# Kernel tuning notes

Measured on AMD Instinct MI355X. Metric: run time of the kernel, lower is better.

The kernel has to match this reference:

```python
import jax, jax.numpy as jnp
import numpy as np

B, D1, T = 256, 512, 256   # batch, input features, time steps
O1, O2 = 256, 128          # output features, output time/classes


def setup_inputs() -> dict:
    key = jax.random.key(0)
    ks = jax.random.split(key, 5)
    x = jax.random.normal(ks[0], (B, D1, T), dtype=jnp.float32)
    W1 = jax.random.normal(ks[1], (O1, D1), dtype=jnp.float32) / np.sqrt(D1).astype(np.float32)
    W = jax.random.normal(ks[2], (T, T), dtype=jnp.float32) / np.sqrt(T).astype(np.float32)
    W2 = jax.random.normal(ks[3], (T, O2), dtype=jnp.float32) / np.sqrt(T).astype(np.float32)
    alpha = jnp.array([0.5], dtype=jnp.float32)
    bias = jax.random.normal(ks[4], (O1, O2), dtype=jnp.float32) * 0.01
    return {"x": x, "W1": W1, "W": W, "W2": W2, "alpha": alpha, "bias": bias}


def reference(x, W1, W, W2, alpha, bias):
    # mode-1 product: project features. E: [B, O1, T]
    E = jnp.einsum('od,bdt->bot', W1, x)
    # temporal attention: softmax over time of E @ W. A: [B, O1, T]
    A = jax.nn.softmax(jnp.einsum('bot,ts->bos', E, W), axis=-1)
    a = alpha[0]
    blended = a * E + (1.0 - a) * E * A
    # mode-2 product: project time axis, add bias. Y: [B, O1, O2]
    Y = jnp.einsum('bot,ts->bos', blended, W2) + bias
    # per-sample softmax over the output-feature axis (torch.softmax(item4[i], 0))
    return jax.nn.softmax(Y, axis=1)
```

## Files before the change

### kernel.cpp

```cpp
#include <hip/hip_runtime.h>
#include <hip/hip_bf16.h>
#include <math.h>

#define B_   256
#define D1_  512
#define T_   256
#define O1_  256
#define O2_  128
#define OT   64

typedef __attribute__((ext_vector_type(8))) _Float16 f16x8;
typedef __attribute__((ext_vector_type(4))) float f32x4;

__device__ inline unsigned pkh2(float a, float b) {
    union { _Float16 h[2]; unsigned u; } c;
    c.h[0] = (_Float16)a; c.h[1] = (_Float16)b; return c.u;
}
__device__ inline uint2 cvth4(float v0, float v1, float v2, float v3) {
    uint2 r; r.x = pkh2(v0, v1); r.y = pkh2(v2, v3); return r;
}
__device__ inline f16x8 cvt8h(const float* v) {
    f16x8 r;
    #pragma unroll
    for (int j = 0; j < 8; ++j) r[j] = (_Float16)v[j];
    return r;
}
__device__ inline f16x8 ld16(const char* p) {
    union { uint2 a[2]; f16x8 v; } f;
    f.a[0] = *(const uint2*)p;
    f.a[1] = *(const uint2*)(p + 8);
    return f.v;
}
__device__ inline f16x8 ldb128(const char* p) { return *(const f16x8*)p; }

#define MFMAH __builtin_amdgcn_mfma_f32_16x16x32_f16

__global__ __launch_bounds__(512, 4) void tabl_mfma(
    const float* __restrict__ x, const float* __restrict__ W1,
    const float* __restrict__ W, const float* __restrict__ W2,
    const float* __restrict__ alpha, const float* __restrict__ bias,
    float* __restrict__ out)
{
    __shared__ __align__(16) char Eh[OT * 512];
    __shared__ __align__(16) char Bst[2][256 * 72];
    __shared__ float redm[4][OT];
    __shared__ float reds[4][OT];

    const int tid    = threadIdx.x;
    const int lane16 = tid & 15;
    const int lg     = (tid >> 4) & 3;
    const int wid    = tid >> 6;
    const int wm     = wid >> 2;
    const int wn     = wid & 3;

    const int bid = blockIdx.x;
    const int idx = bid >> 3;
    const int b     = (bid & 7) + 8 * (idx >> 2);
    const int obase = (idx & 3) * OT;

    const int xs_t  = tid & 255;
    const int xs_kh = tid >> 8;
    const int stO   = xs_t * 72 + xs_kh * 32;
    const int zs = tid & 127, zq = (tid >> 7) & 3;
    const int stZ   = zs * 72 + zq * 16;

    const int rArow[2] = { obase + wm * 32 + lane16, obase + wm * 32 + 16 + lane16 };
    const int eR[2]    = { wm * 32 + lane16, wm * 32 + 16 + lane16 };
    const int eBase[2] = { eR[0] * 512, eR[1] * 512 };
    const int eSw[2]   = { (eR[0] & 7) << 4, (eR[1] & 7) << 4 };
    int bOff[4], b3Off[2];
    #pragma unroll
    for (int nt = 0; nt < 4; ++nt) bOff[nt] = (wn * 64 + nt * 16 + lane16) * 72 + lg * 16;
    #pragma unroll
    for (int nt = 0; nt < 2; ++nt) b3Off[nt] = (wn * 32 + nt * 16 + lane16) * 72 + lg * 16;

    f32x4 Eacc[2][4];
    #pragma unroll
    for (int mt = 0; mt < 2; ++mt)
        #pragma unroll
        for (int nt = 0; nt < 4; ++nt) Eacc[mt][nt] = (f32x4){0.f,0.f,0.f,0.f};

    const float* xcol = x + (size_t)b * (D1_ * T_) + xs_t;
    float xn[16];
    f16x8 AhC[2];

    {
        float x0[16];
        #pragma unroll
        for (int j = 0; j < 16; ++j) x0[j] = xcol[(size_t)(xs_kh * 16 + j) * T_];
        #pragma unroll
        for (int mt = 0; mt < 2; ++mt) {
            float av[8];
            *(float4*)&av[0] = *(const float4*)(W1 + (size_t)rArow[mt] * D1_ + lg * 8);
            *(float4*)&av[4] = *(const float4*)(W1 + (size_t)rArow[mt] * D1_ + lg * 8 + 4);
            AhC[mt] = cvt8h(av);
        }
        #pragma unroll
        for (int q = 0; q < 4; ++q)
            *(uint2*)(Bst[0] + stO + q * 8) = cvth4(x0[q*4+0], x0[q*4+1], x0[q*4+2], x0[q*4+3]);
    }
    __syncthreads();

    #pragma unroll 2
    for (int c = 0; c < 16; ++c) {
        const int cur = c & 1;
        if (c < 15) {
            #pragma unroll
            for (int j = 0; j < 16; ++j)
                xn[j] = xcol[(size_t)((c + 1) * 32 + xs_kh * 16 + j) * T_];
        }
        float4 apN[2][2];
        if (c < 15) {
            #pragma unroll
            for (int mt = 0; mt < 2; ++mt) {
                const float4* ap = (const float4*)(W1 + (size_t)rArow[mt] * D1_ + (c + 1) * 32 + lg * 8);
                apN[mt][0] = ap[0]; apN[mt][1] = ap[1];
            }
        }
        __builtin_amdgcn_s_setprio(1);
        #pragma unroll
        for (int nt = 0; nt < 4; ++nt) {
            f16x8 Bh = ld16(Bst[cur] + bOff[nt]);
            #pragma unroll
            for (int mt = 0; mt < 2; ++mt)
                Eacc[mt][nt] = MFMAH(AhC[mt], Bh, Eacc[mt][nt], 0,0,0);
        }
        __builtin_amdgcn_s_setprio(0);
        if (c < 15) {
            #pragma unroll
            for (int q = 0; q < 4; ++q)
                *(uint2*)(Bst[cur^1] + stO + q * 8) = cvth4(xn[q*4+0], xn[q*4+1], xn[q*4+2], xn[q*4+3]);
            #pragma unroll
            for (int mt = 0; mt < 2; ++mt) {
                float av[8];
                *(float4*)&av[0] = apN[mt][0];
                *(float4*)&av[4] = apN[mt][1];
                AhC[mt] = cvt8h(av);
            }
        }
        __syncthreads();
    }

    #pragma unroll
    for (int mt = 0; mt < 2; ++mt)
        #pragma unroll
        for (int nt = 0; nt < 4; ++nt)
            #pragma unroll
            for (int i = 0; i < 4; ++i) {
                int r = wm * 32 + mt * 16 + lg * 4 + i;
                int t = wn * 64 + nt * 16 + lane16;
                union { _Float16 h; unsigned short u; } cc;
                cc.h = (_Float16)Eacc[mt][nt][i];
                *(unsigned short*)(Eh + r * 512 + ((2 * t) ^ ((r & 7) << 4))) = cc.u;
            }

    f32x4 Sacc[2][4];
    #pragma unroll
    for (int mt = 0; mt < 2; ++mt)
        #pragma unroll
        for (int nt = 0; nt < 4; ++nt) Sacc[mt][nt] = (f32x4){0.f,0.f,0.f,0.f};

    const float* wcol = W + xs_t;
    {
        float w0[16];
        #pragma unroll
        for (int j = 0; j < 16; ++j) w0[j] = wcol[(size_t)(xs_kh * 16 + j) * T_];
        #pragma unroll
        for (int q = 0; q < 4; ++q)
            *(uint2*)(Bst[0] + stO + q * 8) = cvth4(w0[q*4+0], w0[q*4+1], w0[q*4+2], w0[q*4+3]);
    }
    __syncthreads();

    float wv[16];
    #pragma unroll 2
    for (int c = 0; c < 8; ++c) {
        const int cur = c & 1;
        if (c < 7) {
            #pragma unroll
            for (int j = 0; j < 16; ++j)
                wv[j] = wcol[(size_t)((c + 1) * 32 + xs_kh * 16 + j) * T_];
        }
        f16x8 Af[2];
        #pragma unroll
        for (int mt = 0; mt < 2; ++mt)
            Af[mt] = ldb128(Eh + eBase[mt] + ((c * 64 + lg * 16) ^ eSw[mt]));
        __builtin_amdgcn_s_setprio(1);
        #pragma unroll
        for (int nt = 0; nt < 4; ++nt) {
            f16x8 Bf = ld16(Bst[cur] + bOff[nt]);
            #pragma unroll
            for (int mt = 0; mt < 2; ++mt)
                Sacc[mt][nt] = MFMAH(Af[mt], Bf, Sacc[mt][nt], 0,0,0);
        }
        __builtin_amdgcn_s_setprio(0);
        if (c < 7) {
            #pragma unroll
            for (int q = 0; q < 4; ++q)
                *(uint2*)(Bst[cur^1] + stO + q * 8) = cvth4(wv[q*4+0], wv[q*4+1], wv[q*4+2], wv[q*4+3]);
        }
        __syncthreads();
    }

    const float a_ = alpha[0];
    float pm[2][4];
    #pragma unroll
    for (int mt = 0; mt < 2; ++mt)
        #pragma unroll
        for (int i = 0; i < 4; ++i) {
            float m = fmaxf(fmaxf(Sacc[mt][0][i], Sacc[mt][1][i]),
                            fmaxf(Sacc[mt][2][i], Sacc[mt][3][i]));
            m = fmaxf(m, __shfl_xor(m, 1));
            m = fmaxf(m, __shfl_xor(m, 2));
            m = fmaxf(m, __shfl_xor(m, 4));
            m = fmaxf(m, __shfl_xor(m, 8));
            float s = 0.f;
            #pragma unroll
            for (int nt = 0; nt < 4; ++nt) {
                float p = __expf(Sacc[mt][nt][i] - m);
                Sacc[mt][nt][i] = p; s += p;
            }
            s += __shfl_xor(s, 1);
            s += __shfl_xor(s, 2);
            s += __shfl_xor(s, 4);
            s += __shfl_xor(s, 8);
            pm[mt][i] = m;
            if (lane16 == 0) {
                int r = wm * 32 + mt * 16 + lg * 4 + i;
                redm[wn][r] = m; reds[wn][r] = s;
            }
        }
    __syncthreads();

    #pragma unroll
    for (int mt = 0; mt < 2; ++mt)
        #pragma unroll
        for (int i = 0; i < 4; ++i) {
            int r = wm * 32 + mt * 16 + lg * 4 + i;
            float M = fmaxf(fmaxf(redm[0][r], redm[1][r]),
                            fmaxf(redm[2][r], redm[3][r]));
            float den = reds[0][r] * __expf(redm[0][r] - M)
                      + reds[1][r] * __expf(redm[1][r] - M)
                      + reds[2][r] * __expf(redm[2][r] - M)
                      + reds[3][r] * __expf(redm[3][r] - M);
            float sc = __expf(pm[mt][i] - M) / den;
            #pragma unroll
            for (int nt = 0; nt < 4; ++nt) {
                float f = a_ + (1.f - a_) * Sacc[mt][nt][i] * sc;
                int t = wn * 64 + nt * 16 + lane16;
                int off = r * 512 + ((2 * t) ^ ((r & 7) << 4));
                union { _Float16 h; unsigned short u; } cc;
                cc.u = *(const unsigned short*)(Eh + off);
                cc.h = (_Float16)((float)cc.h * f);
                *(unsigned short*)(Eh + off) = cc.u;
            }
        }
    {
        float z0[8];
        #pragma unroll
        for (int j = 0; j < 8; ++j) z0[j] = W2[(size_t)(zq * 8 + j) * O2_ + zs];
        *(uint2*)(Bst[0] + stZ)     = cvth4(z0[0], z0[1], z0[2], z0[3]);
        *(uint2*)(Bst[0] + stZ + 8) = cvth4(z0[4], z0[5], z0[6], z0[7]);
    }
    __syncthreads();

    f32x4 Yacc[2][2];
    #pragma unroll
    for (int mt = 0; mt < 2; ++mt)
        #pragma unroll
        for (int nt = 0; nt < 2; ++nt) Yacc[mt][nt] = (f32x4){0.f,0.f,0.f,0.f};

    float zv[8];
    #pragma unroll 2
    for (int c = 0; c < 8; ++c) {
        const int cur = c & 1;
        if (c < 7) {
            #pragma unroll
            for (int j = 0; j < 8; ++j)
                zv[j] = W2[(size_t)((c + 1) * 32 + zq * 8 + j) * O2_ + zs];
        }
        f16x8 Af[2];
        #pragma unroll
        for (int mt = 0; mt < 2; ++mt)
            Af[mt] = ldb128(Eh + eBase[mt] + ((c * 64 + lg * 16) ^ eSw[mt]));
        __builtin_amdgcn_s_setprio(1);
        #pragma unroll
        for (int nt = 0; nt < 2; ++nt) {
            f16x8 Bf = ld16(Bst[cur] + b3Off[nt]);
            #pragma unroll
            for (int mt = 0; mt < 2; ++mt)
                Yacc[mt][nt] = MFMAH(Af[mt], Bf, Yacc[mt][nt], 0,0,0);
        }
        __builtin_amdgcn_s_setprio(0);
        if (c < 7) {
            *(uint2*)(Bst[cur^1] + stZ)     = cvth4(zv[0], zv[1], zv[2], zv[3]);
            *(uint2*)(Bst[cur^1] + stZ + 8) = cvth4(zv[4], zv[5], zv[6], zv[7]);
        }
        __syncthreads();
    }

    #pragma unroll
    for (int mt = 0; mt < 2; ++mt)
        #pragma unroll
        for (int nt = 0; nt < 2; ++nt)
            #pragma unroll
            for (int i = 0; i < 4; ++i) {
                int o  = obase + wm * 32 + mt * 16 + lg * 4 + i;
                int s2 = wn * 32 + nt * 16 + lane16;
                out[((size_t)b * O1_ + o) * O2_ + s2] =
                    Yacc[mt][nt][i] + bias[(size_t)o * O2_ + s2];
            }
}

__global__ __launch_bounds__(256) void softmax_o1(float* __restrict__ out)
{
    __shared__ float sm[2][128], ss[2][128];
    const int b  = blockIdx.x;
    const int s2 = threadIdx.x & 127;
    const int oh = threadIdx.x >> 7;
    float* p = out + (size_t)b * (O1_ * O2_) + s2;
    float m = -INFINITY, s = 0.f;
    #pragma unroll 4
    for (int o = oh * 128; o < oh * 128 + 128; ++o) {
        float v = p[(size_t)o * O2_];
        float mn = fmaxf(m, v);
        s = s * __expf(m - mn) + __expf(v - mn);
        m = mn;
    }
    sm[oh][s2] = m; ss[oh][s2] = s;
    __syncthreads();
    float M = fmaxf(sm[0][s2], sm[1][s2]);
    float S = ss[0][s2] * __expf(sm[0][s2] - M) + ss[1][s2] * __expf(sm[1][s2] - M);
    float inv = 1.f / S;
    #pragma unroll 4
    for (int o = oh * 128; o < oh * 128 + 128; ++o) {
        float v = p[(size_t)o * O2_];
        p[(size_t)o * O2_] = __expf(v - M) * inv;
    }
}

extern "C" void kernel_launch(void* const* d_in, const int* in_sizes, int n_in,
                              void* d_out, int out_size, void* d_ws, size_t ws_size,
                              hipStream_t stream)
{
    const float* x     = (const float*)d_in[0];
    const float* W1    = (const float*)d_in[1];
    const float* W     = (const float*)d_in[2];
    const float* W2    = (const float*)d_in[3];
    const float* alpha = (const float*)d_in[4];
    const float* bias  = (const float*)d_in[5];
    float* out = (float*)d_out;

    tabl_mfma<<<dim3(1024), 512, 0, stream>>>(x, W1, W, W2, alpha, bias, out);
    softmax_o1<<<B_, 256, 0, stream>>>(out);
}
```

Before: 143.6 us.

## Pre-transpose inputs to fp16 in workspace and load MFMA operands directly from global

```diff
diff --git a/kernel.cpp b/kernel.cpp
--- a/kernel.cpp
+++ b/kernel.cpp
@@ -12,37 +12,79 @@
 typedef __attribute__((ext_vector_type(8))) _Float16 f16x8;
 typedef __attribute__((ext_vector_type(4))) float f32x4;
 
-__device__ inline unsigned pkh2(float a, float b) {
-    union { _Float16 h[2]; unsigned u; } c;
-    c.h[0] = (_Float16)a; c.h[1] = (_Float16)b; return c.u;
-}
-__device__ inline uint2 cvth4(float v0, float v1, float v2, float v3) {
-    uint2 r; r.x = pkh2(v0, v1); r.y = pkh2(v2, v3); return r;
-}
-__device__ inline f16x8 cvt8h(const float* v) {
-    f16x8 r;
-    #pragma unroll
-    for (int j = 0; j < 8; ++j) r[j] = (_Float16)v[j];
-    return r;
-}
-__device__ inline f16x8 ld16(const char* p) {
-    union { uint2 a[2]; f16x8 v; } f;
-    f.a[0] = *(const uint2*)p;
-    f.a[1] = *(const uint2*)(p + 8);
-    return f.v;
-}
+#define MFMAH __builtin_amdgcn_mfma_f32_16x16x32_f16
+
+#define XT_BYTES  (B_ * T_ * D1_ * 2u)
+#define WT_BYTES  (T_ * T_ * 2u)
+#define W2T_BYTES (T_ * O2_ * 2u)
+#define W1H_BYTES (O1_ * D1_ * 2u)
+#define WS_NEED   ((size_t)XT_BYTES + WT_BYTES + W2T_BYTES + W1H_BYTES)
+
 __device__ inline f16x8 ldb128(const char* p) { return *(const f16x8*)p; }
 
-#define MFMAH __builtin_amdgcn_mfma_f32_16x16x32_f16
-
-__global__ __launch_bounds__(512, 4) void tabl_mfma(
-    const float* __restrict__ x, const float* __restrict__ W1,
+__global__ __launch_bounds__(256) void prep_weights(
     const float* __restrict__ W, const float* __restrict__ W2,
+    const float* __restrict__ W1, _Float16* __restrict__ WT,
+    _Float16* __restrict__ W2T, _Float16* __restrict__ W1h)
+{
+    int g = blockIdx.x * 256 + threadIdx.x;
+    if (g < T_ * T_) {
+        int s = g >> 8, t = g & 255;
+        WT[g] = (_Float16)W[t * T_ + s];
+    } else if (g < T_ * T_ + T_ * O2_) {
+        int h = g - T_ * T_;
+        int s2 = h >> 8, t = h & 255;
+        W2T[h] = (_Float16)W2[t * O2_ + s2];
+    } else {
+        int h = g - (T_ * T_ + T_ * O2_);
+        if (h < O1_ * D1_) W1h[h] = (_Float16)W1[h];
+    }
+}
+
+__global__ __launch_bounds__(256) void transpose_x(
+    const float* __restrict__ x, _Float16* __restrict__ xT)
+{
+    __shared__ float tile[64][65];
+    const int bid = blockIdx.x;
+    const int b   = bid >> 5;
+    const int rem = bid & 31;
+    const int d0  = (rem >> 2) * 64;
+    const int t0  = (rem & 3) * 64;
+    const int tid = threadIdx.x;
+
+    {
+        const int j  = tid & 15;
+        const int r0 = tid >> 4;
+        #pragma unroll
+        for (int rr = 0; rr < 4; ++rr) {
+            int dl = r0 + rr * 16;
+            float4 v = *(const float4*)(x + ((size_t)b * D1_ + d0 + dl) * T_ + t0 + j * 4);
+            tile[j * 4 + 0][dl] = v.x;
+            tile[j * 4 + 1][dl] = v.y;
+            tile[j * 4 + 2][dl] = v.z;
+            tile[j * 4 + 3][dl] = v.w;
+        }
+    }
+    __syncthreads();
+    {
+        const int trow = tid >> 2;
+        const int seg  = (tid & 3) * 16;
+        _Float16 h[16];
+        #pragma unroll
+        for (int k = 0; k < 16; ++k) h[k] = (_Float16)tile[trow][seg + k];
+        uint4* dst = (uint4*)(xT + ((size_t)b * T_ + t0 + trow) * D1_ + d0 + seg);
+        dst[0] = ((uint4*)h)[0];
+        dst[1] = ((uint4*)h)[1];
+    }
+}
+
+__global__ __launch_bounds__(512) void tabl_mfma(
+    const _Float16* __restrict__ xT, const _Float16* __restrict__ W1h,
+    const _Float16* __restrict__ WT, const _Float16* __restrict__ W2T,
     const float* __restrict__ alpha, const float* __restrict__ bias,
     float* __restrict__ out)
 {
     __shared__ __align__(16) char Eh[OT * 512];
-    __shared__ __align__(16) char Bst[2][256 * 72];
     __shared__ float redm[4][OT];
     __shared__ float reds[4][OT];
 
@@ -58,21 +100,9 @@
     const int b     = (bid & 7) + 8 * (idx >> 2);
     const int obase = (idx & 3) * OT;
 
-    const int xs_t  = tid & 255;
-    const int xs_kh = tid >> 8;
-    const int stO   = xs_t * 72 + xs_kh * 32;
-    const int zs = tid & 127, zq = (tid >> 7) & 3;
-    const int stZ   = zs * 72 + zq * 16;
-
-    const int rArow[2] = { obase + wm * 32 + lane16, obase + wm * 32 + 16 + lane16 };
     const int eR[2]    = { wm * 32 + lane16, wm * 32 + 16 + lane16 };
     const int eBase[2] = { eR[0] * 512, eR[1] * 512 };
     const int eSw[2]   = { (eR[0] & 7) << 4, (eR[1] & 7) << 4 };
-    int bOff[4], b3Off[2];
-    #pragma unroll
-    for (int nt = 0; nt < 4; ++nt) bOff[nt] = (wn * 64 + nt * 16 + lane16) * 72 + lg * 16;
-    #pragma unroll
-    for (int nt = 0; nt < 2; ++nt) b3Off[nt] = (wn * 32 + nt * 16 + lane16) * 72 + lg * 16;
 
     f32x4 Eacc[2][4];
     #pragma unroll
@@ -80,66 +110,50 @@
         #pragma unroll
         for (int nt = 0; nt < 4; ++nt) Eacc[mt][nt] = (f32x4){0.f,0.f,0.f,0.f};
 
-    const float* xcol = x + (size_t)b * (D1_ * T_) + xs_t;
-    float xn[16];
-    f16x8 AhC[2];
-
-    {
-        float x0[16];
-        #pragma unroll
-        for (int j = 0; j < 16; ++j) x0[j] = xcol[(size_t)(xs_kh * 16 + j) * T_];
-        #pragma unroll
-        for (int mt = 0; mt < 2; ++mt) {
-            float av[8];
-            *(float4*)&av[0] = *(const float4*)(W1 + (size_t)rArow[mt] * D1_ + lg * 8);
-            *(float4*)&av[4] = *(const float4*)(W1 + (size_t)rArow[mt] * D1_ + lg * 8 + 4);
-            AhC[mt] = cvt8h(av);
-        }
-        #pragma unroll
-        for (int q = 0; q < 4; ++q)
-            *(uint2*)(Bst[0] + stO + q * 8) = cvth4(x0[q*4+0], x0[q*4+1], x0[q*4+2], x0[q*4+3]);
-    }
-    __syncthreads();
+    const _Float16* xTb = xT + (size_t)b * T_ * D1_;
+    const _Float16* aB[2] = {
+        W1h + (size_t)(obase + eR[0]) * D1_ + lg * 8,
+        W1h + (size_t)(obase + eR[1]) * D1_ + lg * 8 };
+    const _Float16* bB[4];
+    #pragma unroll
+    for (int nt = 0; nt < 4; ++nt)
+        bB[nt] = xTb + (size_t)(wn * 64 + nt * 16 + lane16) * D1_ + lg * 8;
+
+    f16x8 Bpf[4], Apf[2];
+    #pragma unroll
+    for (int nt = 0; nt < 4; ++nt) Bpf[nt] = *(const f16x8*)bB[nt];
+    Apf[0] = *(const f16x8*)aB[0];
+    Apf[1] = *(const f16x8*)aB[1];
 
     #pragma unroll 2
     for (int c = 0; c < 16; ++c) {
-        const int cur = c & 1;
+        f16x8 Bc[4], Ac[2];
+        #pragma unroll
+        for (int nt = 0; nt < 4; ++nt) Bc[nt] = Bpf[nt];
+        Ac[0] = Apf[0]; Ac[1] = Apf[1];
         if (c < 15) {
             #pragma unroll
-            for (int j = 0; j < 16; ++j)
-                xn[j] = xcol[(size_t)((c + 1) * 32 + xs_kh * 16 + j) * T_];
-        }
-        float4 apN[2][2];
-        if (c < 15) {
-            #pragma unroll
-            for (int mt = 0; mt < 2; ++mt) {
-                const float4* ap = (const float4*)(W1 + (size_t)rArow[mt] * D1_ + (c + 1) * 32 + lg * 8);
-                apN[mt][0] = ap[0]; apN[mt][1] = ap[1];
-            }
+            for (int nt = 0; nt < 4; ++nt)
+                Bpf[nt] = *(const f16x8*)(bB[nt] + (c + 1) * 32);
+            Apf[0] = *(const f16x8*)(aB[0] + (c + 1) * 32);
+            Apf[1] = *(const f16x8*)(aB[1] + (c + 1) * 32);
         }
         __builtin_amdgcn_s_setprio(1);
         #pragma unroll
-        for (int nt = 0; nt < 4; ++nt) {
-            f16x8 Bh = ld16(Bst[cur] + bOff[nt]);
+        for (int nt = 0; nt < 4; ++nt)
             #pragma unroll
             for (int mt = 0; mt < 2; ++mt)
-                Eacc[mt][nt] = MFMAH(AhC[mt], Bh, Eacc[mt][nt], 0,0,0);
-        }
+                Eacc[mt][nt] = MFMAH(Ac[mt], Bc[nt], Eacc[mt][nt], 0,0,0);
         __builtin_amdgcn_s_setprio(0);
-        if (c < 15) {
-            #pragma unroll
-            for (int q = 0; q < 4; ++q)
-                *(uint2*)(Bst[cur^1] + stO + q * 8) = cvth4(xn[q*4+0], xn[q*4+1], xn[q*4+2], xn[q*4+3]);
-            #pragma unroll
-            for (int mt = 0; mt < 2; ++mt) {
-                float av[8];
-                *(float4*)&av[0] = apN[mt][0];
-                *(float4*)&av[4] = apN[mt][1];
-                AhC[mt] = cvt8h(av);
-            }
-        }
-        __syncthreads();
-    }
+    }
+
+    const _Float16* wB[4];
+    #pragma unroll
+    for (int nt = 0; nt < 4; ++nt)
+        wB[nt] = WT + (size_t)(wn * 64 + nt * 16 + lane16) * T_ + lg * 8;
+    f16x8 Wpf[4];
+    #pragma unroll
+    for (int nt = 0; nt < 4; ++nt) Wpf[nt] = *(const f16x8*)wB[nt];
 
     #pragma unroll
     for (int mt = 0; mt < 2; ++mt)
@@ -153,6 +167,7 @@
                 cc.h = (_Float16)Eacc[mt][nt][i];
                 *(unsigned short*)(Eh + r * 512 + ((2 * t) ^ ((r & 7) << 4))) = cc.u;
             }
+    __syncthreads();
 
     f32x4 Sacc[2][4];
     #pragma unroll
@@ -160,45 +175,27 @@
         #pragma unroll
         for (int nt = 0; nt < 4; ++nt) Sacc[mt][nt] = (f32x4){0.f,0.f,0.f,0.f};
 
-    const float* wcol = W + xs_t;
-    {
-        float w0[16];
-        #pragma unroll
-        for (int j = 0; j < 16; ++j) w0[j] = wcol[(size_t)(xs_kh * 16 + j) * T_];
-        #pragma unroll
-        for (int q = 0; q < 4; ++q)
-            *(uint2*)(Bst[0] + stO + q * 8) = cvth4(w0[q*4+0], w0[q*4+1], w0[q*4+2], w0[q*4+3]);
-    }
-    __syncthreads();
-
-    float wv[16];
     #pragma unroll 2
     for (int c = 0; c < 8; ++c) {
-        const int cur = c & 1;
-        if (c < 7) {
-            #pragma unroll
-            for (int j = 0; j < 16; ++j)
-                wv[j] = wcol[(size_t)((c + 1) * 32 + xs_kh * 16 + j) * T_];
-        }
         f16x8 Af[2];
         #pragma unroll
         for (int mt = 0; mt < 2; ++mt)
             Af[mt] = ldb128(Eh + eBase[mt] + ((c * 64 + lg * 16) ^ eSw[mt]));
+        f16x8 Bc[4];
+        #pragma unroll
+        for (int nt = 0; nt < 4; ++nt) Bc[nt] = Wpf[nt];
+        if (c < 7) {
+            #pragma unroll
+            for (int nt = 0; nt < 4; ++nt)
+                Wpf[nt] = *(const f16x8*)(wB[nt] + (c + 1) * 32);
+        }
         __builtin_amdgcn_s_setprio(1);
         #pragma unroll
-        for (int nt = 0; nt < 4; ++nt) {
-            f16x8 Bf = ld16(Bst[cur] + bOff[nt]);
+        for (int nt = 0; nt < 4; ++nt)
             #pragma unroll
             for (int mt = 0; mt < 2; ++mt)
-                Sacc[mt][nt] = MFMAH(Af[mt], Bf, Sacc[mt][nt], 0,0,0);
-        }
+                Sacc[mt][nt] = MFMAH(Af[mt], Bc[nt], Sacc[mt][nt], 0,0,0);
         __builtin_amdgcn_s_setprio(0);
-        if (c < 7) {
-            #pragma unroll
-            for (int q = 0; q < 4; ++q)
-                *(uint2*)(Bst[cur^1] + stO + q * 8) = cvth4(wv[q*4+0], wv[q*4+1], wv[q*4+2], wv[q*4+3]);
-        }
-        __syncthreads();
     }
 
     const float a_ = alpha[0];
@@ -254,13 +251,12 @@
                 *(unsigned short*)(Eh + off) = cc.u;
             }
         }
-    {
-        float z0[8];
-        #pragma unroll
-        for (int j = 0; j < 8; ++j) z0[j] = W2[(size_t)(zq * 8 + j) * O2_ + zs];
-        *(uint2*)(Bst[0] + stZ)     = cvth4(z0[0], z0[1], z0[2], z0[3]);
-        *(uint2*)(Bst[0] + stZ + 8) = cvth4(z0[4], z0[5], z0[6], z0[7]);
-    }
+    const _Float16* zB[2] = {
+        W2T + (size_t)(wn * 32 + lane16) * T_ + lg * 8,
+        W2T + (size_t)(wn * 32 + 16 + lane16) * T_ + lg * 8 };
+    f16x8 Zpf[2];
+    Zpf[0] = *(const f16x8*)zB[0];
+    Zpf[1] = *(const f16x8*)zB[1];
     __syncthreads();
 
     f32x4 Yacc[2][2];
@@ -269,33 +265,24 @@
         #pragma unroll
         for (int nt = 0; nt < 2; ++nt) Yacc[mt][nt] = (f32x4){0.f,0.f,0.f,0.f};
 
-    float zv[8];
     #pragma unroll 2
     for (int c = 0; c < 8; ++c) {
-        const int cur = c & 1;
-        if (c < 7) {
-            #pragma unroll
-            for (int j = 0; j < 8; ++j)
-                zv[j] = W2[(size_t)((c + 1) * 32 + zq * 8 + j) * O2_ + zs];
-        }
         f16x8 Af[2];
         #pragma unroll
         for (int mt = 0; mt < 2; ++mt)
             Af[mt] = ldb128(Eh + eBase[mt] + ((c * 64 + lg * 16) ^ eSw[mt]));
+        f16x8 Bc[2] = { Zpf[0], Zpf[1] };
+        if (c < 7) {
+            Zpf[0] = *(const f16x8*)(zB[0] + (c + 1) * 32);
+            Zpf[1] = *(const f16x8*)(zB[1] + (c + 1) * 32);
+        }
         __builtin_amdgcn_s_setprio(1);
         #pragma unroll
-        for (int nt = 0; nt < 2; ++nt) {
-            f16x8 Bf = ld16(Bst[cur] + b3Off[nt]);
+        for (int nt = 0; nt < 2; ++nt)
             #pragma unroll
             for (int mt = 0; mt < 2; ++mt)
-                Yacc[mt][nt] = MFMAH(Af[mt], Bf, Yacc[mt][nt], 0,0,0);
-        }
+                Yacc[mt][nt] = MFMAH(Af[mt], Bc[nt], Yacc[mt][nt], 0,0,0);
         __builtin_amdgcn_s_setprio(0);
-        if (c < 7) {
-            *(uint2*)(Bst[cur^1] + stZ)     = cvth4(zv[0], zv[1], zv[2], zv[3]);
-            *(uint2*)(Bst[cur^1] + stZ + 8) = cvth4(zv[4], zv[5], zv[6], zv[7]);
-        }
-        __syncthreads();
     }
 
     #pragma unroll
@@ -350,6 +337,16 @@
     const float* bias  = (const float*)d_in[5];
     float* out = (float*)d_out;
 
-    tabl_mfma<<<dim3(1024), 512, 0, stream>>>(x, W1, W, W2, alpha, bias, out);
+    if (ws_size < WS_NEED) return;
+
+    char* ws = (char*)d_ws;
+    _Float16* xT  = (_Float16*)ws;
+    _Float16* WT  = (_Float16*)(ws + XT_BYTES);
+    _Float16* W2T = (_Float16*)(ws + XT_BYTES + WT_BYTES);
+    _Float16* W1h = (_Float16*)(ws + XT_BYTES + WT_BYTES + W2T_BYTES);
+
+    prep_weights<<<dim3(896), 256, 0, stream>>>(W, W2, W1, WT, W2T, W1h);
+    transpose_x<<<dim3(8192), 256, 0, stream>>>(x, xT);
+    tabl_mfma<<<dim3(1024), 512, 0, stream>>>(xT, W1h, WT, W2T, alpha, bias, out);
     softmax_o1<<<B_, 256, 0, stream>>>(out);
 }
```

Result: slower. 196.4 us (+36.8%).
